# Performance work log

Measured on AMD Instinct MI355X. Metric: run time of the kernel, lower is better.

The kernel has to match this reference:

```python
import jax, jax.numpy as jnp
import numpy as np

HEADS = 16
DIM_HEAD = 64
RMS_EPS = 1.1920929e-07  # torch.finfo(float32).eps (torch RMSNorm eps=None default)
ROPE_THETA = 10000.0


def _rope(x):
    # x: [b, h, n, d]; rotary-embedding-torch style interleaved rotation
    n, d = x.shape[-2], x.shape[-1]
    inv_freq = 1.0 / (ROPE_THETA ** (jnp.arange(0, d, 2, dtype=jnp.float32) / d))
    t = jnp.arange(n, dtype=jnp.float32)
    freqs = t[:, None] * inv_freq[None, :]              # [n, d/2]
    cos = jnp.repeat(jnp.cos(freqs), 2, axis=-1)        # [n, d] interleaved
    sin = jnp.repeat(jnp.sin(freqs), 2, axis=-1)
    x1 = x[..., ::2]
    x2 = x[..., 1::2]
    rot = jnp.stack((-x2, x1), axis=-1).reshape(x.shape)  # rotate_half, interleaved pairs
    return x * cos + rot * sin


def setup_inputs() -> dict:
    key = jax.random.key(0)
    ks = jax.random.split(key, 6)
    b, n, dim = 2, 2048, 1024
    tokens = jax.random.normal(ks[0], (b, n, dim), dtype=jnp.float32)
    norm_weight = jnp.ones((dim,), dtype=jnp.float32)
    wq = jax.random.normal(ks[1], (dim, dim), dtype=jnp.float32) * 0.02
    wk = jax.random.normal(ks[2], (dim, dim), dtype=jnp.float32) * 0.02
    wv = jax.random.normal(ks[3], (dim, dim), dtype=jnp.float32) * 0.02
    wo = jax.random.normal(ks[4], (dim, dim), dtype=jnp.float32) * 0.02
    return {"tokens": tokens, "norm_weight": norm_weight, "wq": wq, "wk": wk, "wv": wv, "wo": wo}


def reference(tokens, norm_weight, wq, wk, wv, wo):
    b, n, dim = tokens.shape
    # RMSNorm (elementwise affine)
    x = tokens * jax.lax.rsqrt(jnp.mean(tokens * tokens, axis=-1, keepdims=True) + RMS_EPS)
    x = x * norm_weight
    # QKV projections (torch Linear: x @ W.T), split heads: b n (h d) -> b h n d
    def split(y):
        return y.reshape(b, n, HEADS, DIM_HEAD).transpose(0, 2, 1, 3)
    q = split(x @ wq.T) * (DIM_HEAD ** -0.5)
    k = split(x @ wk.T)
    v = split(x @ wv.T)
    # rotary embedding (no kv cache -> same positions for q and k)
    q = _rope(q)
    k = _rope(k)
    sim = jnp.einsum('bhid,bhjd->bhij', q, k)
    causal = jnp.triu(jnp.ones((n, n), dtype=bool), k=1)
    sim = jnp.where(causal, -jnp.finfo(sim.dtype).max, sim)
    attn = jax.nn.softmax(sim, axis=-1)
    out = jnp.einsum('bhij,bhjd->bhid', attn, v)
    out = out.transpose(0, 2, 1, 3).reshape(b, n, dim)  # merge heads
    return out @ wo.T
```

## Files before the change

### kernel.cpp

```cpp
#include <hip/hip_runtime.h>

typedef __bf16 bf16x8 __attribute__((ext_vector_type(8)));
typedef float f32x4 __attribute__((ext_vector_type(4)));

#define DIM 1024
#define NSEQ 2048

#define GL2LDS(g, l) __builtin_amdgcn_global_load_lds( \
    (const __attribute__((address_space(1))) void*)(g), \
    (__attribute__((address_space(3))) void*)(l), 16, 0, 0)

#define MFMA16(a, b, c) __builtin_amdgcn_mfma_f32_16x16x32_bf16(a, b, c, 0, 0, 0)

__global__ __launch_bounds__(256) void cvt_kernel(const float* __restrict__ s,
                                                  __bf16* __restrict__ d) {
    int i = (blockIdx.x * 256 + threadIdx.x) * 4;
    float4 f = *(const float4*)(s + i);
    union { uint2 u; __bf16 h[4]; } p;
    p.h[0] = (__bf16)f.x; p.h[1] = (__bf16)f.y;
    p.h[2] = (__bf16)f.z; p.h[3] = (__bf16)f.w;
    *(uint2*)(d + i) = p.u;
}

__global__ __launch_bounds__(256) void cvt3_kernel(const float* __restrict__ wq,
                                                   const float* __restrict__ wk,
                                                   const float* __restrict__ wv,
                                                   __bf16* __restrict__ dq,
                                                   __bf16* __restrict__ dk,
                                                   __bf16* __restrict__ dv,
                                                   int* __restrict__ counters) {
    if (blockIdx.x == 0 && blockIdx.y == 0 && threadIdx.x < 8)
        counters[threadIdx.x] = 0;
    const float* s = blockIdx.y == 0 ? wq : (blockIdx.y == 1 ? wk : wv);
    __bf16*      d = blockIdx.y == 0 ? dq : (blockIdx.y == 1 ? dk : dv);
    int i = (blockIdx.x * 256 + threadIdx.x) * 4;
    float4 f = *(const float4*)(s + i);
    union { uint2 u; __bf16 h[4]; } p;
    p.h[0] = (__bf16)f.x; p.h[1] = (__bf16)f.y;
    p.h[2] = (__bf16)f.z; p.h[3] = (__bf16)f.w;
    *(uint2*)(d + i) = p.u;
}

__global__ __launch_bounds__(256) void rmsnorm_kernel(const float* __restrict__ x,
                                                      const float* __restrict__ g,
                                                      __bf16* __restrict__ o) {
    int row = blockIdx.x;
    int t = threadIdx.x;
    float4 xv = ((const float4*)(x + (size_t)row * DIM))[t];
    float ss = xv.x*xv.x + xv.y*xv.y + xv.z*xv.z + xv.w*xv.w;
    #pragma unroll
    for (int off = 32; off; off >>= 1) ss += __shfl_xor(ss, off, 64);
    __shared__ float red[4];
    if ((t & 63) == 0) red[t >> 6] = ss;
    __syncthreads();
    ss = red[0] + red[1] + red[2] + red[3];
    float r = rsqrtf(ss * (1.0f / 1024.0f) + 1.1920929e-07f);
    float4 gv = ((const float4*)g)[t];
    union { uint2 u; __bf16 h[4]; } p;
    p.h[0] = (__bf16)(xv.x * r * gv.x);
    p.h[1] = (__bf16)(xv.y * r * gv.y);
    p.h[2] = (__bf16)(xv.z * r * gv.z);
    p.h[3] = (__bf16)(xv.w * r * gv.w);
    *(uint2*)(o + (size_t)row * DIM + t * 4) = p.u;
}

__global__ __launch_bounds__(256) void rope_kernel(__bf16* __restrict__ qb,
                                                   __bf16* __restrict__ kb) {
    int bid = blockIdx.x;
    __bf16* x = (bid & 1) ? kb : qb;
    int gid = (bid >> 1) * 256 + threadIdx.x;
    int row = gid >> 9;
    int pr = gid & 511;
    int pos = row & (NSEQ - 1);
    int dp = pr & 31;
    float inv = __expf(-(float)dp * (9.210340371976184f / 32.0f));
    float ang = (float)pos * inv;
    float sn, cs;
    sincosf(ang, &sn, &cs);
    size_t off = (size_t)row * DIM + pr * 2;
    union { unsigned int u; __bf16 h[2]; } p;
    p.u = *(const unsigned int*)(x + off);
    float x1 = (float)p.h[0], x2 = (float)p.h[1];
    p.h[0] = (__bf16)(x1 * cs - x2 * sn);
    p.h[1] = (__bf16)(x2 * cs + x1 * sn);
    *(unsigned int*)(x + off) = p.u;
}

template <typename CT>
__device__ __forceinline__ void gemm_body(const __bf16* __restrict__ A,
                                          const __bf16* __restrict__ B,
                                          CT* __restrict__ C,
                                          int mb, int nb, int ldc, float scale,
                                          __bf16* As, __bf16* Bs) {
    int t = threadIdx.x;
    int w = t >> 6, l = t & 63;
    int wm = (w >> 1) * 64, wn = (w & 1) * 64;
    int lrow = l & 15, lq = l >> 4;
    f32x4 acc[4][4] = {};

    int srow = w * 32 + (l >> 3);
    int sc8 = (l & 7) * 8;
    const __bf16* gA = A + (size_t)(mb * 128 + srow) * 1024 + sc8;
    const __bf16* gB = B + (size_t)(nb * 128 + srow) * 1024 + sc8;
    __bf16* lA = As + (size_t)(w * 32) * 64;
    __bf16* lB = Bs + (size_t)(w * 32) * 64;

    for (int kt = 0; kt < 16; ++kt) {
        int k0 = kt * 64;
        #pragma unroll
        for (int c = 0; c < 4; ++c) {
            GL2LDS(gA + (size_t)c * 8 * 1024 + k0, lA + c * 8 * 64);
            GL2LDS(gB + (size_t)c * 8 * 1024 + k0, lB + c * 8 * 64);
        }
        __syncthreads();
        #pragma unroll
        for (int ch = 0; ch < 2; ++ch) {
            bf16x8 af[4], bfr[4];
            #pragma unroll
            for (int i = 0; i < 4; ++i)
                af[i] = *(const bf16x8*)&As[(wm + i * 16 + lrow) * 64 + ch * 32 + lq * 8];
            #pragma unroll
            for (int i = 0; i < 4; ++i)
                bfr[i] = *(const bf16x8*)&Bs[(wn + i * 16 + lrow) * 64 + ch * 32 + lq * 8];
            #pragma unroll
            for (int rt = 0; rt < 4; ++rt)
                #pragma unroll
                for (int ct = 0; ct < 4; ++ct)
                    acc[rt][ct] = MFMA16(af[rt], bfr[ct], acc[rt][ct]);
        }
        __syncthreads();
    }
    #pragma unroll
    for (int rt = 0; rt < 4; ++rt)
        #pragma unroll
        for (int ct = 0; ct < 4; ++ct)
            #pragma unroll
            for (int r = 0; r < 4; ++r) {
                int row = mb * 128 + wm + rt * 16 + lq * 4 + r;
                int col = nb * 128 + wn + ct * 16 + lrow;
                C[(size_t)row * ldc + col] = (CT)(acc[rt][ct][r] * scale);
            }
}

__global__ __launch_bounds__(256) void qkv_kernel(const __bf16* __restrict__ x,
                                                  const __bf16* __restrict__ wq,
                                                  const __bf16* __restrict__ wk,
                                                  const __bf16* __restrict__ wv,
                                                  __bf16* __restrict__ qb,
                                                  __bf16* __restrict__ kb,
                                                  __bf16* __restrict__ vtb) {
    __shared__ __bf16 As[128 * 64];
    __shared__ __bf16 Bs[128 * 64];
    int bm = blockIdx.x, bn = blockIdx.y, z = blockIdx.z;
    if (z == 0)      gemm_body<__bf16>(x,  wq, qb,  bm, bn, 1024,
                                       0.125f * 1.44269504088896340736f, As, Bs);
    else if (z == 1) gemm_body<__bf16>(x,  wk, kb,  bm, bn, 1024, 1.0f,   As, Bs);
    else             gemm_body<__bf16>(wv, x,  vtb, bn, bm, 4096, 1.0f,   As, Bs);
}

__global__ __launch_bounds__(256) void wo_kernel(const __bf16* __restrict__ A,
                                                 const __bf16* __restrict__ B,
                                                 float* __restrict__ C) {
    __shared__ __bf16 As[128 * 64];
    __shared__ __bf16 Bs[128 * 64];
    gemm_body<float>(A, B, C, blockIdx.x, blockIdx.y, 1024, 1.0f, As, Bs);
}

__global__ __launch_bounds__(256) void attn_kernel(const __bf16* __restrict__ q,
                                                   const __bf16* __restrict__ kk,
                                                   const __bf16* __restrict__ vt,
                                                   __bf16* __restrict__ o,
                                                   int* __restrict__ counters) {
    int xcd = blockIdx.x & 7;
    int t = threadIdx.x;
    int w = t >> 6, l = t & 63;
    int lrow = l & 15, lq = l >> 4;
    int row0 = t >> 3;
    int c8 = (t & 7) * 8;

    __shared__ __bf16 Kt[2][64 * 72];
    __shared__ __bf16 Vs[2][64 * 72];
    __shared__ __bf16 Ps[4][32 * 76];
    __shared__ int s_item;
    __bf16* pw = Ps[w];

    for (;;) {
        if (t == 0) s_item = atomicAdd(&counters[xcd], 1);
        __syncthreads();
        int item = s_item;
        if (item >= 64) break;
        int qt = 15 - (item >> 2);
        int bh = xcd * 4 + (item & 3);
        int h = bh & 15;
        int b = bh >> 4;
        int rowbase = b * NSEQ;
        int JT = 2 * qt + 1;

        const __bf16* kbase = kk + (size_t)rowbase * DIM + h * 64;
        const __bf16* vbase = vt + (size_t)(h * 64) * 4096 + b * 2048;

        bf16x8 qf[2][2];
        #pragma unroll
        for (int g = 0; g < 2; ++g) {
            const __bf16* qp = q + (size_t)(rowbase + qt * 128 + w * 32 + g * 16 + lrow) * DIM + h * 64;
            qf[g][0] = *(const bf16x8*)(qp + lq * 8);
            qf[g][1] = *(const bf16x8*)(qp + 32 + lq * 8);
        }

        f32x4 oacc[2][4] = {};
        float m_r[2] = {-1e30f, -1e30f};
        float l_r[2] = {0.0f, 0.0f};

        uint4 kr0, kr1, vr0, vr1;
        kr0 = *(const uint4*)(kbase + (size_t)row0 * DIM + c8);
        kr1 = *(const uint4*)(kbase + (size_t)(row0 + 32) * DIM + c8);
        vr0 = *(const uint4*)(vbase + (size_t)row0 * 4096 + c8);
        vr1 = *(const uint4*)(vbase + (size_t)(row0 + 32) * 4096 + c8);
        *(uint4*)&Kt[0][row0 * 72 + c8] = kr0;
        *(uint4*)&Kt[0][(row0 + 32) * 72 + c8] = kr1;
        *(uint4*)&Vs[0][row0 * 72 + c8] = vr0;
        *(uint4*)&Vs[0][(row0 + 32) * 72 + c8] = vr1;
        __syncthreads();

        for (int jt = 0; jt <= JT; ++jt) {
            int cur = jt & 1;
            if (jt < JT) {
                int j0 = (jt + 1) * 64;
                kr0 = *(const uint4*)(kbase + (size_t)(j0 + row0) * DIM + c8);
                kr1 = *(const uint4*)(kbase + (size_t)(j0 + row0 + 32) * DIM + c8);
                vr0 = *(const uint4*)(vbase + (size_t)row0 * 4096 + j0 + c8);
                vr1 = *(const uint4*)(vbase + (size_t)(row0 + 32) * 4096 + j0 + c8);
            }
            f32x4 st[2][4];
            #pragma unroll
            for (int ct = 0; ct < 4; ++ct) {
                bf16x8 ka0 = *(const bf16x8*)&Kt[cur][(ct * 16 + lrow) * 72 + lq * 8];
                bf16x8 ka1 = *(const bf16x8*)&Kt[cur][(ct * 16 + lrow) * 72 + 32 + lq * 8];
                #pragma unroll
                for (int g = 0; g < 2; ++g) {
                    f32x4 z = {};
                    z = MFMA16(ka0, qf[g][0], z);
                    z = MFMA16(ka1, qf[g][1], z);
                    st[g][ct] = z;
                }
            }
            if (jt >= JT - 1) {
                #pragma unroll
                for (int g = 0; g < 2; ++g) {
                    int qrel = qt * 128 + w * 32 + g * 16 + lrow - jt * 64;
                    #pragma unroll
                    for (int ct = 0; ct < 4; ++ct)
                        #pragma unroll
                        for (int r = 0; r < 4; ++r)
                            if (ct * 16 + lq * 4 + r > qrel) st[g][ct][r] = -3.0e38f;
                }
            }
            #pragma unroll
            for (int g = 0; g < 2; ++g) {
                float m0 = fmaxf(fmaxf(st[g][0][0], st[g][0][1]), fmaxf(st[g][0][2], st[g][0][3]));
                float m1 = fmaxf(fmaxf(st[g][1][0], st[g][1][1]), fmaxf(st[g][1][2], st[g][1][3]));
                float m2 = fmaxf(fmaxf(st[g][2][0], st[g][2][1]), fmaxf(st[g][2][2], st[g][2][3]));
                float m3 = fmaxf(fmaxf(st[g][3][0], st[g][3][1]), fmaxf(st[g][3][2], st[g][3][3]));
                float mx = fmaxf(fmaxf(m0, m1), fmaxf(m2, m3));
                mx = fmaxf(mx, __shfl_xor(mx, 16, 64));
                mx = fmaxf(mx, __shfl_xor(mx, 32, 64));
                if (!__all(mx - m_r[g] <= 8.0f)) {
                    float mnew = fmaxf(m_r[g], mx);
                    float alpha = __builtin_amdgcn_exp2f(m_r[g] - mnew);
                    l_r[g] *= alpha;
                    #pragma unroll
                    for (int ct = 0; ct < 4; ++ct)
                        #pragma unroll
                        for (int r = 0; r < 4; ++r) oacc[g][ct][r] *= alpha;
                    m_r[g] = mnew;
                }
                float ps = 0.0f;
                #pragma unroll
                for (int ct = 0; ct < 4; ++ct)
                    #pragma unroll
                    for (int r = 0; r < 4; ++r) {
                        float p = __builtin_amdgcn_exp2f(st[g][ct][r] - m_r[g]);
                        st[g][ct][r] = p;
                        ps += p;
                    }
                ps += __shfl_xor(ps, 16, 64);
                ps += __shfl_xor(ps, 32, 64);
                l_r[g] += ps;
            }
            #pragma unroll
            for (int g = 0; g < 2; ++g)
                #pragma unroll
                for (int ct = 0; ct < 4; ++ct) {
                    union { uint2 u; __bf16 h4[4]; } pk;
                    #pragma unroll
                    for (int r = 0; r < 4; ++r) pk.h4[r] = (__bf16)st[g][ct][r];
                    *(uint2*)&pw[(g * 16 + lrow) * 76 + ct * 16 + lq * 4] = pk.u;
                }
            bf16x8 pb[2][2];
            #pragma unroll
            for (int g = 0; g < 2; ++g) {
                pb[g][0] = *(const bf16x8*)&pw[(g * 16 + lrow) * 76 + lq * 8];
                pb[g][1] = *(const bf16x8*)&pw[(g * 16 + lrow) * 76 + 32 + lq * 8];
            }
            #pragma unroll
            for (int ct = 0; ct < 4; ++ct) {
                bf16x8 va0 = *(const bf16x8*)&Vs[cur][(ct * 16 + lrow) * 72 + lq * 8];
                bf16x8 va1 = *(const bf16x8*)&Vs[cur][(ct * 16 + lrow) * 72 + 32 + lq * 8];
                #pragma unroll
                for (int g = 0; g < 2; ++g) {
                    oacc[g][ct] = MFMA16(va0, pb[g][0], oacc[g][ct]);
                    oacc[g][ct] = MFMA16(va1, pb[g][1], oacc[g][ct]);
                }
            }
            if (jt < JT) {
                *(uint4*)&Kt[cur ^ 1][row0 * 72 + c8] = kr0;
                *(uint4*)&Kt[cur ^ 1][(row0 + 32) * 72 + c8] = kr1;
                *(uint4*)&Vs[cur ^ 1][row0 * 72 + c8] = vr0;
                *(uint4*)&Vs[cur ^ 1][(row0 + 32) * 72 + c8] = vr1;
            }
            __syncthreads();
        }
        #pragma unroll
        for (int g = 0; g < 2; ++g) {
            float rcp = 1.0f / l_r[g];
            const size_t orow = (size_t)(rowbase + qt * 128 + w * 32 + g * 16 + lrow) * DIM + h * 64;
            #pragma unroll
            for (int ct = 0; ct < 4; ++ct) {
                union { uint2 u; __bf16 h4[4]; } pk;
                #pragma unroll
                for (int r = 0; r < 4; ++r) pk.h4[r] = (__bf16)(oacc[g][ct][r] * rcp);
                *(uint2*)(o + orow + ct * 16 + lq * 4) = pk.u;
            }
        }
    }
}

extern "C" void kernel_launch(void* const* d_in, const int* in_sizes, int n_in,
                              void* d_out, int out_size, void* d_ws, size_t ws_size,
                              hipStream_t stream) {
    const float* tokens = (const float*)d_in[0];
    const float* gamma  = (const float*)d_in[1];
    const float* wq = (const float*)d_in[2];
    const float* wk = (const float*)d_in[3];
    const float* wv = (const float*)d_in[4];
    const float* wo = (const float*)d_in[5];

    __bf16* ws  = (__bf16*)d_ws;
    __bf16* x   = ws;
    __bf16* qb  = x   + (size_t)4096 * 1024;
    __bf16* kb  = qb  + (size_t)4096 * 1024;
    __bf16* vtb = kb  + (size_t)4096 * 1024;
    __bf16* ao  = x;
    __bf16* wob = qb;
    float*  out = (float*)d_out;

    __bf16* wqb = (__bf16*)d_out;
    __bf16* wkb = wqb + (size_t)1024 * 1024;
    __bf16* wvb = wkb + (size_t)1024 * 1024;
    int* counters = (int*)((char*)d_out + (size_t)8 * 1024 * 1024);

    cvt3_kernel<<<dim3(1024, 3), 256, 0, stream>>>(wq, wk, wv, wqb, wkb, wvb, counters);

    rmsnorm_kernel<<<4096, 256, 0, stream>>>(tokens, gamma, x);

    qkv_kernel<<<dim3(32, 8, 3), 256, 0, stream>>>(x, wqb, wkb, wvb, qb, kb, vtb);

    rope_kernel<<<16384, 256, 0, stream>>>(qb, kb);

    attn_kernel<<<256, 256, 0, stream>>>(qb, kb, vtb, ao, counters);

    cvt_kernel<<<1024, 256, 0, stream>>>(wo, wob);

    wo_kernel<<<dim3(32, 8), 256, 0, stream>>>(ao, wob, out);
}
```

Baseline: 234.5 us.

## Split attention KV range across wave pairs with smaller query tiles and merge

Attention work items shrink from 128 to 64 query rows, giving 128 items per XCD. The four waves split into two row groups times two KV-parity groups that process alternating 64-key tiles, then merge their partial softmax states through LDS at the end. LDS tiles become unpadded with an XOR swizzle, launch bounds request 3 blocks per CU and the grid grows to 768. This aims at better load balance and occupancy on the causal workload, at the cost of extra syncs and a final reduction step.

```diff
diff --git a/kernel.cpp b/kernel.cpp
--- a/kernel.cpp
+++ b/kernel.cpp
@@ -166,21 +166,23 @@
     gemm_body<float>(A, B, C, blockIdx.x, blockIdx.y, 1024, 1.0f, As, Bs);
 }
 
-__global__ __launch_bounds__(256) void attn_kernel(const __bf16* __restrict__ q,
-                                                   const __bf16* __restrict__ kk,
-                                                   const __bf16* __restrict__ vt,
-                                                   __bf16* __restrict__ o,
-                                                   int* __restrict__ counters) {
+__global__ __launch_bounds__(256, 3) void attn_kernel(const __bf16* __restrict__ q,
+                                                      const __bf16* __restrict__ kk,
+                                                      const __bf16* __restrict__ vt,
+                                                      __bf16* __restrict__ o,
+                                                      int* __restrict__ counters) {
     int xcd = blockIdx.x & 7;
     int t = threadIdx.x;
     int w = t >> 6, l = t & 63;
     int lrow = l & 15, lq = l >> 4;
+    int rw = (w & 1) * 32;
+    int par = w >> 1;
     int row0 = t >> 3;
-    int c8 = (t & 7) * 8;
-
-    __shared__ __bf16 Kt[2][64 * 72];
-    __shared__ __bf16 Vs[2][64 * 72];
-    __shared__ __bf16 Ps[4][32 * 76];
+    int cb = t & 7;
+
+    __shared__ __bf16 Kt[2][64 * 64];
+    __shared__ __bf16 Vs[2][64 * 64];
+    __shared__ __bf16 Ps[4][32 * 72];
     __shared__ int s_item;
     __bf16* pw = Ps[w];
 
@@ -188,13 +190,12 @@
         if (t == 0) s_item = atomicAdd(&counters[xcd], 1);
         __syncthreads();
         int item = s_item;
-        if (item >= 64) break;
-        int qt = 15 - (item >> 2);
+        if (item >= 128) break;
+        int iq = 31 - (item >> 2);
         int bh = xcd * 4 + (item & 3);
         int h = bh & 15;
         int b = bh >> 4;
         int rowbase = b * NSEQ;
-        int JT = 2 * qt + 1;
 
         const __bf16* kbase = kk + (size_t)rowbase * DIM + h * 64;
         const __bf16* vbase = vt + (size_t)(h * 64) * 4096 + b * 2048;
@@ -202,7 +203,7 @@
         bf16x8 qf[2][2];
         #pragma unroll
         for (int g = 0; g < 2; ++g) {
-            const __bf16* qp = q + (size_t)(rowbase + qt * 128 + w * 32 + g * 16 + lrow) * DIM + h * 64;
+            const __bf16* qp = q + (size_t)(rowbase + iq * 64 + rw + g * 16 + lrow) * DIM + h * 64;
             qf[g][0] = *(const bf16x8*)(qp + lq * 8);
             qf[g][1] = *(const bf16x8*)(qp + 32 + lq * 8);
         }
@@ -211,125 +212,179 @@
         float m_r[2] = {-1e30f, -1e30f};
         float l_r[2] = {0.0f, 0.0f};
 
-        uint4 kr0, kr1, vr0, vr1;
-        kr0 = *(const uint4*)(kbase + (size_t)row0 * DIM + c8);
-        kr1 = *(const uint4*)(kbase + (size_t)(row0 + 32) * DIM + c8);
-        vr0 = *(const uint4*)(vbase + (size_t)row0 * 4096 + c8);
-        vr1 = *(const uint4*)(vbase + (size_t)(row0 + 32) * 4096 + c8);
-        *(uint4*)&Kt[0][row0 * 72 + c8] = kr0;
-        *(uint4*)&Kt[0][(row0 + 32) * 72 + c8] = kr1;
-        *(uint4*)&Vs[0][row0 * 72 + c8] = vr0;
-        *(uint4*)&Vs[0][(row0 + 32) * 72 + c8] = vr1;
-        __syncthreads();
-
-        for (int jt = 0; jt <= JT; ++jt) {
-            int cur = jt & 1;
-            if (jt < JT) {
-                int j0 = (jt + 1) * 64;
-                kr0 = *(const uint4*)(kbase + (size_t)(j0 + row0) * DIM + c8);
-                kr1 = *(const uint4*)(kbase + (size_t)(j0 + row0 + 32) * DIM + c8);
-                vr0 = *(const uint4*)(vbase + (size_t)row0 * 4096 + j0 + c8);
-                vr1 = *(const uint4*)(vbase + (size_t)(row0 + 32) * 4096 + j0 + c8);
+        const __bf16* kg = kbase + (size_t)row0 * DIM + cb * 8;
+        const __bf16* vg = vbase + (size_t)row0 * 4096 + cb * 8;
+        int dsw0 = (row0 * 8 + (cb ^ (row0 & 7))) * 8;
+        int dsw1 = ((row0 + 32) * 8 + (cb ^ (row0 & 7))) * 8;
+
+        uint4 k0a, k0b, v0a, v0b, k1a, k1b, v1a, v1b;
+        k0a = *(const uint4*)(kg);
+        k0b = *(const uint4*)(kg + (size_t)32 * DIM);
+        v0a = *(const uint4*)(vg);
+        v0b = *(const uint4*)(vg + (size_t)32 * 4096);
+        if (iq >= 1) {
+            k1a = *(const uint4*)(kg + (size_t)64 * DIM);
+            k1b = *(const uint4*)(kg + (size_t)96 * DIM);
+            v1a = *(const uint4*)(vg + 64);
+            v1b = *(const uint4*)(vg + (size_t)32 * 4096 + 64);
+        }
+        *(uint4*)&Kt[0][dsw0] = k0a; *(uint4*)&Kt[0][dsw1] = k0b;
+        *(uint4*)&Vs[0][dsw0] = v0a; *(uint4*)&Vs[0][dsw1] = v0b;
+        if (iq >= 1) {
+            *(uint4*)&Kt[1][dsw0] = k1a; *(uint4*)&Kt[1][dsw1] = k1b;
+            *(uint4*)&Vs[1][dsw0] = v1a; *(uint4*)&Vs[1][dsw1] = v1b;
+        }
+        __syncthreads();
+
+        int R = (iq + 2) >> 1;
+        for (int rd = 0; rd < R; ++rd) {
+            int jt = 2 * rd + par;
+            bool pf = (rd + 1 < R);
+            if (pf) {
+                int je = 2 * rd + 2;
+                size_t ko = (size_t)je * 64 * DIM;
+                k0a = *(const uint4*)(kg + ko);
+                k0b = *(const uint4*)(kg + ko + (size_t)32 * DIM);
+                v0a = *(const uint4*)(vg + je * 64);
+                v0b = *(const uint4*)(vg + (size_t)32 * 4096 + je * 64);
+                if (je + 1 <= iq) {
+                    k1a = *(const uint4*)(kg + ko + (size_t)64 * DIM);
+                    k1b = *(const uint4*)(kg + ko + (size_t)96 * DIM);
+                    v1a = *(const uint4*)(vg + je * 64 + 64);
+                    v1b = *(const uint4*)(vg + (size_t)32 * 4096 + je * 64 + 64);
+                }
             }
-            f32x4 st[2][4];
-            #pragma unroll
-            for (int ct = 0; ct < 4; ++ct) {
-                bf16x8 ka0 = *(const bf16x8*)&Kt[cur][(ct * 16 + lrow) * 72 + lq * 8];
-                bf16x8 ka1 = *(const bf16x8*)&Kt[cur][(ct * 16 + lrow) * 72 + 32 + lq * 8];
+            if (jt <= iq) {
+                const __bf16* Kb = Kt[par];
+                const __bf16* Vb = Vs[par];
+                int sw = lrow & 7;
+                f32x4 st[2][4];
+                #pragma unroll
+                for (int ct = 0; ct < 4; ++ct) {
+                    int rr = (ct * 16 + lrow) * 8;
+                    bf16x8 ka0 = *(const bf16x8*)&Kb[(rr + (lq ^ sw)) * 8];
+                    bf16x8 ka1 = *(const bf16x8*)&Kb[(rr + ((4 + lq) ^ sw)) * 8];
+                    #pragma unroll
+                    for (int g = 0; g < 2; ++g) {
+                        f32x4 z = {};
+                        z = MFMA16(ka0, qf[g][0], z);
+                        z = MFMA16(ka1, qf[g][1], z);
+                        st[g][ct] = z;
+                    }
+                }
+                if (jt == iq) {
+                    #pragma unroll
+                    for (int g = 0; g < 2; ++g) {
+                        int qrel = rw + g * 16 + lrow;
+                        #pragma unroll
+                        for (int ct = 0; ct < 4; ++ct)
+                            #pragma unroll
+                            for (int r = 0; r < 4; ++r)
+                                if (ct * 16 + lq * 4 + r > qrel) st[g][ct][r] = -3.0e38f;
+                    }
+                }
                 #pragma unroll
                 for (int g = 0; g < 2; ++g) {
-                    f32x4 z = {};
-                    z = MFMA16(ka0, qf[g][0], z);
-                    z = MFMA16(ka1, qf[g][1], z);
-                    st[g][ct] = z;
-                }
-            }
-            if (jt >= JT - 1) {
-                #pragma unroll
-                for (int g = 0; g < 2; ++g) {
-                    int qrel = qt * 128 + w * 32 + g * 16 + lrow - jt * 64;
+                    float m0 = fmaxf(fmaxf(st[g][0][0], st[g][0][1]), fmaxf(st[g][0][2], st[g][0][3]));
+                    float m1 = fmaxf(fmaxf(st[g][1][0], st[g][1][1]), fmaxf(st[g][1][2], st[g][1][3]));
+                    float m2 = fmaxf(fmaxf(st[g][2][0], st[g][2][1]), fmaxf(st[g][2][2], st[g][2][3]));
+                    float m3 = fmaxf(fmaxf(st[g][3][0], st[g][3][1]), fmaxf(st[g][3][2], st[g][3][3]));
+                    float mx = fmaxf(fmaxf(m0, m1), fmaxf(m2, m3));
+                    mx = fmaxf(mx, __shfl_xor(mx, 16, 64));
+                    mx = fmaxf(mx, __shfl_xor(mx, 32, 64));
+                    if (!__all(mx - m_r[g] <= 8.0f)) {
+                        float mnew = fmaxf(m_r[g], mx);
+                        float alpha = __builtin_amdgcn_exp2f(m_r[g] - mnew);
+                        l_r[g] *= alpha;
+                        #pragma unroll
+                        for (int ct = 0; ct < 4; ++ct)
+                            #pragma unroll
+                            for (int r = 0; r < 4; ++r) oacc[g][ct][r] *= alpha;
+                        m_r[g] = mnew;
+                    }
+                    float ps = 0.0f;
                     #pragma unroll
                     for (int ct = 0; ct < 4; ++ct)
                         #pragma unroll
-                        for (int r = 0; r < 4; ++r)
-                            if (ct * 16 + lq * 4 + r > qrel) st[g][ct][r] = -3.0e38f;
+                        for (int r = 0; r < 4; ++r) {
+                            float p = __builtin_amdgcn_exp2f(st[g][ct][r] - m_r[g]);
+                            st[g][ct][r] = p;
+                            ps += p;
+                        }
+                    ps += __shfl_xor(ps, 16, 64);
+                    ps += __shfl_xor(ps, 32, 64);
+                    l_r[g] += ps;
+                }
+                #pragma unroll
+                for (int g = 0; g < 2; ++g)
+                    #pragma unroll
+                    for (int ct = 0; ct < 4; ++ct) {
+                        union { uint2 u; __bf16 h4[4]; } pk;
+                        #pragma unroll
+                        for (int r = 0; r < 4; ++r) pk.h4[r] = (__bf16)st[g][ct][r];
+                        *(uint2*)&pw[(g * 16 + lrow) * 72 + ct * 16 + lq * 4] = pk.u;
+                    }
+                bf16x8 pb[2][2];
+                #pragma unroll
+                for (int g = 0; g < 2; ++g) {
+                    pb[g][0] = *(const bf16x8*)&pw[(g * 16 + lrow) * 72 + lq * 8];
+                    pb[g][1] = *(const bf16x8*)&pw[(g * 16 + lrow) * 72 + 32 + lq * 8];
+                }
+                #pragma unroll
+                for (int ct = 0; ct < 4; ++ct) {
+                    int rr = (ct * 16 + lrow) * 8;
+                    bf16x8 va0 = *(const bf16x8*)&Vb[(rr + (lq ^ sw)) * 8];
+                    bf16x8 va1 = *(const bf16x8*)&Vb[(rr + ((4 + lq) ^ sw)) * 8];
+                    #pragma unroll
+                    for (int g = 0; g < 2; ++g) {
+                        oacc[g][ct] = MFMA16(va0, pb[g][0], oacc[g][ct]);
+                        oacc[g][ct] = MFMA16(va1, pb[g][1], oacc[g][ct]);
+                    }
                 }
             }
+            if (pf) {
+                __syncthreads();
+                *(uint4*)&Kt[0][dsw0] = k0a; *(uint4*)&Kt[0][dsw1] = k0b;
+                *(uint4*)&Vs[0][dsw0] = v0a; *(uint4*)&Vs[0][dsw1] = v0b;
+                if (2 * rd + 3 <= iq) {
+                    *(uint4*)&Kt[1][dsw0] = k1a; *(uint4*)&Kt[1][dsw1] = k1b;
+                    *(uint4*)&Vs[1][dsw0] = v1a; *(uint4*)&Vs[1][dsw1] = v1b;
+                }
+                __syncthreads();
+            }
+        }
+
+        __syncthreads();
+        float* sc = (float*)&Ps[0][0];
+        float* base = sc + (w & 1) * 2304 + l * 36;
+        if (par == 1) {
+            #pragma unroll
+            for (int g = 0; g < 2; ++g)
+                #pragma unroll
+                for (int ct = 0; ct < 4; ++ct)
+                    *(f32x4*)(base + g * 16 + ct * 4) = oacc[g][ct];
+            base[32] = m_r[0]; base[33] = m_r[1];
+            base[34] = l_r[0]; base[35] = l_r[1];
+        }
+        __syncthreads();
+        if (par == 0) {
             #pragma unroll
             for (int g = 0; g < 2; ++g) {
-                float m0 = fmaxf(fmaxf(st[g][0][0], st[g][0][1]), fmaxf(st[g][0][2], st[g][0][3]));
-                float m1 = fmaxf(fmaxf(st[g][1][0], st[g][1][1]), fmaxf(st[g][1][2], st[g][1][3]));
-                float m2 = fmaxf(fmaxf(st[g][2][0], st[g][2][1]), fmaxf(st[g][2][2], st[g][2][3]));
-                float m3 = fmaxf(fmaxf(st[g][3][0], st[g][3][1]), fmaxf(st[g][3][2], st[g][3][3]));
-                float mx = fmaxf(fmaxf(m0, m1), fmaxf(m2, m3));
-                mx = fmaxf(mx, __shfl_xor(mx, 16, 64));
-                mx = fmaxf(mx, __shfl_xor(mx, 32, 64));
-                if (!__all(mx - m_r[g] <= 8.0f)) {
-                    float mnew = fmaxf(m_r[g], mx);
-                    float alpha = __builtin_amdgcn_exp2f(m_r[g] - mnew);
-                    l_r[g] *= alpha;
-                    #pragma unroll
-                    for (int ct = 0; ct < 4; ++ct)
-                        #pragma unroll
-                        for (int r = 0; r < 4; ++r) oacc[g][ct][r] *= alpha;
-                    m_r[g] = mnew;
-                }
-                float ps = 0.0f;
-                #pragma unroll
-                for (int ct = 0; ct < 4; ++ct)
-                    #pragma unroll
-                    for (int r = 0; r < 4; ++r) {
-                        float p = __builtin_amdgcn_exp2f(st[g][ct][r] - m_r[g]);
-                        st[g][ct][r] = p;
-                        ps += p;
-                    }
-                ps += __shfl_xor(ps, 16, 64);
-                ps += __shfl_xor(ps, 32, 64);
-                l_r[g] += ps;
-            }
-            #pragma unroll
-            for (int g = 0; g < 2; ++g)
+                float mb = base[32 + g], lb = base[34 + g];
+                float m = fmaxf(m_r[g], mb);
+                float a  = __builtin_amdgcn_exp2f(m_r[g] - m);
+                float bb = __builtin_amdgcn_exp2f(mb - m);
+                float rcp = 1.0f / (a * l_r[g] + bb * lb);
+                const size_t orow = (size_t)(rowbase + iq * 64 + rw + g * 16 + lrow) * DIM + h * 64;
                 #pragma unroll
                 for (int ct = 0; ct < 4; ++ct) {
+                    f32x4 ob = *(const f32x4*)(base + g * 16 + ct * 4);
                     union { uint2 u; __bf16 h4[4]; } pk;
                     #pragma unroll
-                    for (int r = 0; r < 4; ++r) pk.h4[r] = (__bf16)st[g][ct][r];
-                    *(uint2*)&pw[(g * 16 + lrow) * 76 + ct * 16 + lq * 4] = pk.u;
-                }
-            bf16x8 pb[2][2];
-            #pragma unroll
-            for (int g = 0; g < 2; ++g) {
-                pb[g][0] = *(const bf16x8*)&pw[(g * 16 + lrow) * 76 + lq * 8];
-                pb[g][1] = *(const bf16x8*)&pw[(g * 16 + lrow) * 76 + 32 + lq * 8];
-            }
-            #pragma unroll
-            for (int ct = 0; ct < 4; ++ct) {
-                bf16x8 va0 = *(const bf16x8*)&Vs[cur][(ct * 16 + lrow) * 72 + lq * 8];
-                bf16x8 va1 = *(const bf16x8*)&Vs[cur][(ct * 16 + lrow) * 72 + 32 + lq * 8];
-                #pragma unroll
-                for (int g = 0; g < 2; ++g) {
-                    oacc[g][ct] = MFMA16(va0, pb[g][0], oacc[g][ct]);
-                    oacc[g][ct] = MFMA16(va1, pb[g][1], oacc[g][ct]);
-                }
-            }
-            if (jt < JT) {
-                *(uint4*)&Kt[cur ^ 1][row0 * 72 + c8] = kr0;
-                *(uint4*)&Kt[cur ^ 1][(row0 + 32) * 72 + c8] = kr1;
-                *(uint4*)&Vs[cur ^ 1][row0 * 72 + c8] = vr0;
-                *(uint4*)&Vs[cur ^ 1][(row0 + 32) * 72 + c8] = vr1;
-            }
-            __syncthreads();
-        }
-        #pragma unroll
-        for (int g = 0; g < 2; ++g) {
-            float rcp = 1.0f / l_r[g];
-            const size_t orow = (size_t)(rowbase + qt * 128 + w * 32 + g * 16 + lrow) * DIM + h * 64;
-            #pragma unroll
-            for (int ct = 0; ct < 4; ++ct) {
-                union { uint2 u; __bf16 h4[4]; } pk;
-                #pragma unroll
-                for (int r = 0; r < 4; ++r) pk.h4[r] = (__bf16)(oacc[g][ct][r] * rcp);
-                *(uint2*)(o + orow + ct * 16 + lq * 4) = pk.u;
+                    for (int r = 0; r < 4; ++r)
+                        pk.h4[r] = (__bf16)((a * oacc[g][ct][r] + bb * ob[r]) * rcp);
+                    *(uint2*)(o + orow + ct * 16 + lq * 4) = pk.u;
+                }
             }
         }
     }
@@ -367,7 +422,7 @@
 
     rope_kernel<<<16384, 256, 0, stream>>>(qb, kb);
 
-    attn_kernel<<<256, 256, 0, stream>>>(qb, kb, vtb, ao, counters);
+    attn_kernel<<<768, 256, 0, stream>>>(qb, kb, vtb, ao, counters);
 
     cvt_kernel<<<1024, 256, 0, stream>>>(wo, wob);
 
```

New measurement: 201.8 us. 14.0% less time.
